# Optimization experiments

Hardware: AMD Instinct MI355X
Metric: run time of the kernel (lower is better)

The kernel has to match this reference:

```python
import jax, jax.numpy as jnp
import numpy as np

B, S, D = 2, 2048, 1024
H, KS = 16, 64

def setup_inputs() -> dict:
    key = jax.random.key(0)
    k1, k2, k3, k4, k5 = jax.random.split(key, 5)
    return {
        "x": jax.random.normal(k1, (B, S, D), dtype=jnp.float32),
        "Wq": jax.random.normal(k2, (D, KS, H), dtype=jnp.float32) * 0.02,
        "Wk": jax.random.normal(k3, (D, KS, H), dtype=jnp.float32) * 0.02,
        "Wv": jax.random.normal(k4, (D, KS, H), dtype=jnp.float32) * 0.02,
        "kernel": jax.random.normal(k5, (H * KS, KS), dtype=jnp.float32) * 0.02,
    }

def reference(x, Wq, Wk, Wv, kernel):
    b, s, d = x.shape
    ks, h = Wq.shape[1], Wq.shape[2]
    # projections: heads-last layout [b, s, ks, h]
    q = jnp.einsum('bsd,dkh->bskh', x, Wq)
    k = jnp.einsum('bsd,dkh->bskh', x, Wk)
    v = jnp.einsum('bsd,dkh->bskh', x, Wv)
    # scores [b, i(query), l(key), h]
    scores = jnp.einsum('bikh,blkh->bilh', q, k) / jnp.sqrt(jnp.float32(ks))
    # strictly-upper-triangular (future) mask, as in the original:
    # band_part(ones,0,-1) - eye  ->  1 where l > i
    li = jnp.arange(s)
    mask = (li[None, :] > li[:, None]).astype(jnp.float32)  # [s, s]
    scores = scores - 1e8 * mask[None, :, :, None]
    weights = jax.nn.softmax(scores, axis=2)  # softmax over key axis l
    heads = jnp.einsum('bilh,blkh->bikh', weights, v)  # [b, s, ks, h]
    heads = heads.reshape(b, s, ks * h)  # row-major flatten of (ks, h), matching tf.reshape
    return heads @ kernel  # [b, s, ks]
```

## Files before the change

### kernel.cpp

```cpp
#include <hip/hip_runtime.h>
#include <hip/hip_bf16.h>

#define BB 2
#define SS 2048
#define DD 1024
#define HH 16
#define KSZ 64

typedef __attribute__((ext_vector_type(8))) short s16x8;
typedef __attribute__((ext_vector_type(4))) short s16x4;
typedef __attribute__((ext_vector_type(4))) float f32x4;
typedef __attribute__((ext_vector_type(8))) unsigned short u16x8;
typedef __attribute__((ext_vector_type(4))) unsigned short u16x4;
typedef __attribute__((ext_vector_type(2))) unsigned int u32x2;
typedef unsigned short u16;

__device__ __forceinline__ u16 bf16rne(float f) {
  unsigned int u = __float_as_uint(f);
  unsigned int r = (u + 0x7FFFu + ((u >> 16) & 1u)) >> 16;
  return (u16)r;
}

__device__ __forceinline__ unsigned int cvtpk_bf16(float lo, float hi) {
  unsigned int r;
  asm("v_cvt_pk_bf16_f32 %0, %1, %2" : "=v"(r) : "v"(lo), "v"(hi));
  return r;
}

#if __has_builtin(__builtin_amdgcn_mfma_f32_16x16x16_bf16)
__device__ __forceinline__ f32x4 mfma16(s16x4 a, s16x4 b, f32x4 c) {
  return __builtin_amdgcn_mfma_f32_16x16x16_bf16(a, b, c, 0, 0, 0);
}
#elif __has_builtin(__builtin_amdgcn_mfma_f32_16x16x16bf16_1k)
__device__ __forceinline__ f32x4 mfma16(s16x4 a, s16x4 b, f32x4 c) {
  return __builtin_amdgcn_mfma_f32_16x16x16bf16_1k(a, b, c, 0, 0, 0);
}
#else
__device__ __forceinline__ f32x4 mfma16(s16x4 a, s16x4 b, f32x4 c) {
  asm("s_nop 1\n\tv_mfma_f32_16x16x16_bf16 %0, %1, %2, %0"
      : "+v"(c) : "v"(a), "v"(b));
  return c;
}
#endif

__device__ __forceinline__ void lds_dma16(const u16* g, u16* l) {
  __builtin_amdgcn_global_load_lds(
      (const __attribute__((address_space(1))) unsigned int*)(const void*)g,
      (__attribute__((address_space(3))) unsigned int*)(void*)l, 16, 0, 0);
}

__global__ __launch_bounds__(256) void prep_all(
    const float* __restrict__ x, const float* __restrict__ Wq,
    const float* __restrict__ Wk, const float* __restrict__ Wv,
    const float* __restrict__ kern, u16* __restrict__ xb,
    u16* __restrict__ Wt, u16* __restrict__ BpT) {
  __shared__ float Ts[64][65];
  const int bid = blockIdx.x;
  const int tid = threadIdx.x;
  if (bid < 2048) {
    int idx = (bid * 256 + tid) * 8;
    float4 a = *(const float4*)(x + idx);
    float4 b = *(const float4*)(x + idx + 4);
    u16x8 v;
    v[0] = bf16rne(a.x); v[1] = bf16rne(a.y); v[2] = bf16rne(a.z); v[3] = bf16rne(a.w);
    v[4] = bf16rne(b.x); v[5] = bf16rne(b.y); v[6] = bf16rne(b.z); v[7] = bf16rne(b.w);
    *(u16x8*)(xb + idx) = v;
  } else if (bid < 2816) {
    const int bx = bid - 2048;
    const int p = bx >> 8, rem = bx & 255;
    const int d0 = (rem & 15) * 64, n0 = (rem >> 4) * 64;
    const float* W = (p == 0) ? Wq : (p == 1) ? Wk : Wv;
    u16* Wo = Wt + (size_t)p * DD * DD;
    #pragma unroll
    for (int i = 0; i < 4; ++i) {
      int f4 = tid + i * 256;
      int r = f4 >> 4, c4 = f4 & 15;
      float4 v = *(const float4*)(W + (size_t)(d0 + r) * DD + n0 + c4 * 4);
      Ts[r][c4 * 4 + 0] = v.x; Ts[r][c4 * 4 + 1] = v.y;
      Ts[r][c4 * 4 + 2] = v.z; Ts[r][c4 * 4 + 3] = v.w;
    }
    __syncthreads();
    #pragma unroll
    for (int i = 0; i < 4; ++i) {
      int ch = tid + i * 256;
      int n = ch >> 4, d4 = ch & 15;
      u16x4 o;
      #pragma unroll
      for (int j = 0; j < 4; ++j) o[j] = bf16rne(Ts[d4 * 4 + j][n]);
      *(u16x4*)(Wo + (size_t)(n0 + n) * DD + d0 + d4 * 4) = o;
    }
  } else {
    const int n = bid - 2816;
    const int k4 = tid * 4;
    u16x4 o;
    #pragma unroll
    for (int j = 0; j < 4; ++j) {
      int kp = k4 + j;
      int h = kp >> 6, k = kp & 63;
      o[j] = bf16rne(kern[(size_t)(k * HH + h) * KSZ + n]);
    }
    *(u16x4*)(BpT + (size_t)n * (HH * KSZ) + k4) = o;
  }
}

__global__ __launch_bounds__(512, 6) void proj_kernel(
    const u16* __restrict__ xb, const u16* __restrict__ Wt,
    u16* __restrict__ qkvT) {
  const int xcd = blockIdx.x & 7;
  const int idx = blockIdx.x >> 3;
  const int mt = (xcd >> 1) * 8 + (idx & 7);
  const int nt = (xcd & 1) * 4 + ((idx >> 3) & 3);
  const int p  = idx >> 5;
  const int m0 = mt * 128, n0 = nt * 128;
  const u16* W = Wt + (size_t)p * DD * DD;
  u16* outp = qkvT + (size_t)p * (BB * HH * SS * KSZ);

  __shared__ __align__(16) unsigned char raw[49152];
  u16* lds = (u16*)raw;
  u16* Cs  = (u16*)raw;

  const int tid = threadIdx.x;
  const int wave = tid >> 6, lane = tid & 63;
  const int g = lane >> 4, c = lane & 15;
  const int mbase = (wave & 1) * 64, nbase = (wave >> 1) * 32;

  const int lr = lane >> 2, lc = lane & 3;
  const int swz = (lc ^ ((lr >> 1) & 3)) * 8;
  const int rS = wave * 16;
  const u16* srcA = xb + (size_t)(m0 + rS + lr) * DD + swz;
  const u16* srcB = W  + (size_t)(n0 + rS + lr) * DD + swz;
  const int sl = rS * 32;

  f32x4 acc[4][2];
  #pragma unroll
  for (int i = 0; i < 4; ++i)
    #pragma unroll
    for (int j = 0; j < 2; ++j) acc[i][j] = {0.f, 0.f, 0.f, 0.f};

  {
    u16* A0 = lds;                u16* B0 = lds + 4096;
    u16* A1 = lds + 8192;         u16* B1 = lds + 8192 + 4096;
    lds_dma16(srcA, A0 + sl);       lds_dma16(srcB, B0 + sl);
    lds_dma16(srcA + 32, A1 + sl);  lds_dma16(srcB + 32, B1 + sl);
  }

  const int jsw = (c >> 1) & 3;
  int cr = 0;
  #pragma unroll 1
  for (int t = 0; t < 31; ++t) {
    asm volatile("s_waitcnt vmcnt(2)" ::: "memory");
    __builtin_amdgcn_s_barrier();
    __builtin_amdgcn_sched_barrier(0);
    if (t <= 29) {
      const int st = cr ? cr - 1 : 2;
      const int ko = (t + 2) * 32;
      u16* An = lds + st * 8192;
      u16* Bn = An + 4096;
      lds_dma16(srcA + ko, An + sl);  lds_dma16(srcB + ko, Bn + sl);
    }
    u16* Ac = lds + cr * 8192;
    u16* Bc = Ac + 4096;
    s16x8 af[4], bfr[2];
    #pragma unroll
    for (int mf = 0; mf < 4; ++mf)
      af[mf] = *(const s16x8*)&Ac[(mbase + mf * 16 + c) * 32 + ((g ^ jsw) * 8)];
    #pragma unroll
    for (int nf = 0; nf < 2; ++nf)
      bfr[nf] = *(const s16x8*)&Bc[(nbase + nf * 16 + c) * 32 + ((g ^ jsw) * 8)];
    #pragma unroll
    for (int mf = 0; mf < 4; ++mf)
      #pragma unroll
      for (int nf = 0; nf < 2; ++nf)
        acc[mf][nf] = __builtin_amdgcn_mfma_f32_16x16x32_bf16(
            af[mf], bfr[nf], acc[mf][nf], 0, 0, 0);
    cr = (cr >= 2) ? 0 : cr + 1;
  }
  asm volatile("s_waitcnt vmcnt(0)" ::: "memory");
  __builtin_amdgcn_s_barrier();
  __builtin_amdgcn_sched_barrier(0);
  {
    u16* Ac = lds + cr * 8192;
    u16* Bc = Ac + 4096;
    s16x8 af[4], bfr[2];
    #pragma unroll
    for (int mf = 0; mf < 4; ++mf)
      af[mf] = *(const s16x8*)&Ac[(mbase + mf * 16 + c) * 32 + ((g ^ jsw) * 8)];
    #pragma unroll
    for (int nf = 0; nf < 2; ++nf)
      bfr[nf] = *(const s16x8*)&Bc[(nbase + nf * 16 + c) * 32 + ((g ^ jsw) * 8)];
    #pragma unroll
    for (int mf = 0; mf < 4; ++mf)
      #pragma unroll
      for (int nf = 0; nf < 2; ++nf)
        acc[mf][nf] = __builtin_amdgcn_mfma_f32_16x16x32_bf16(
            af[mf], bfr[nf], acc[mf][nf], 0, 0, 0);
  }
  __syncthreads();

  const float cscale = (p == 0) ? 0.125f * 1.44269504f : 1.0f;
  #pragma unroll
  for (int mf = 0; mf < 4; ++mf)
    #pragma unroll
    for (int nf = 0; nf < 2; ++nf)
      #pragma unroll
      for (int r = 0; r < 4; ++r)
        Cs[(mbase + mf * 16 + g * 4 + r) * 136 + nbase + nf * 16 + c] =
            bf16rne(acc[mf][nf][r] * cscale);
  __syncthreads();
  const int b = m0 >> 11;
  if (p < 2) {
    int hh = tid >> 5, s5 = tid & 31;
    #pragma unroll
    for (int i = 0; i < 4; ++i) {
      int row = i * 32 + s5;
      int s = (m0 + row) & 2047;
      u16x8 v;
      #pragma unroll
      for (int kp = 0; kp < 8; ++kp) v[kp] = Cs[row * 136 + kp * 16 + hh];
      *(u16x8*)(outp + ((size_t)(b * HH + hh) * SS + s) * KSZ + (n0 >> 4)) = v;
    }
  } else {
    const int s0 = m0 & 2047;
    #pragma unroll
    for (int i = 0; i < 4; ++i) {
      int chunk = tid + i * 512;
      int colid = chunk >> 4;
      int hh = colid >> 3, kp = colid & 7;
      int s8 = chunk & 15;
      u16x8 v;
      #pragma unroll
      for (int j = 0; j < 8; ++j) v[j] = Cs[(s8 * 8 + j) * 136 + kp * 16 + hh];
      *(u16x8*)(outp + ((size_t)(b * HH + hh) * KSZ + (n0 >> 4) + kp) * SS +
                s0 + s8 * 8) = v;
    }
  }
}

__global__ __launch_bounds__(256, 2) void attn_kernel(
    const u16* __restrict__ qkvT, u16* __restrict__ headsB) {
  const int bid = blockIdx.x;
  const int hb = bid & 31;
  const int q5 = bid >> 5;
  const int qt = (q5 < 8) ? q5 : 23 - q5;
  const int h = hb & 15, b = hb >> 4;
  const size_t plane = (size_t)(b * HH + h) * SS * KSZ;
  const size_t PSZ = (size_t)BB * HH * SS * KSZ;
  const u16* Qg = qkvT + plane;
  const u16* Kg = qkvT + PSZ + plane;
  const u16* Vg = qkvT + 2 * PSZ + plane;

  __shared__ u16 Ks[2][64 * 64];
  __shared__ u16 Vt[2][64 * 64];

  const int tid = threadIdx.x;
  const int lane = tid & 63;
  const int g = lane >> 4, c = lane & 15;
  const int wq0 = (tid >> 6) * 32;
  const int sr = tid >> 3, sc = tid & 7;
  const int soA = sr * 64 + ((sc ^ (sr & 7)) * 8);
  const int soB = soA + 32 * 64;

  const int nt = 2 * qt + 2;

  s16x8 bq[2][2];
  #pragma unroll
  for (int sq = 0; sq < 2; ++sq) {
    const size_t qrow = (size_t)(qt * 128 + wq0 + sq * 16 + c) * KSZ;
    bq[sq][0] = *(const s16x8*)(Qg + qrow + g * 8);
    bq[sq][1] = *(const s16x8*)(Qg + qrow + 32 + g * 8);
  }

  u16x8 kr0 = *(const u16x8*)(Kg + (size_t)sr * KSZ + sc * 8);
  u16x8 kr1 = *(const u16x8*)(Kg + (size_t)(sr + 32) * KSZ + sc * 8);
  u16x8 vr0 = *(const u16x8*)(Vg + (size_t)sr * SS + sc * 8);
  u16x8 vr1 = *(const u16x8*)(Vg + (size_t)(sr + 32) * SS + sc * 8);
  *(u16x8*)&Ks[0][soA] = kr0; *(u16x8*)&Ks[0][soB] = kr1;
  *(u16x8*)&Vt[0][soA] = vr0; *(u16x8*)&Vt[0][soB] = vr1;
  kr0 = *(const u16x8*)(Kg + (size_t)(64 + sr) * KSZ + sc * 8);
  kr1 = *(const u16x8*)(Kg + (size_t)(64 + sr + 32) * KSZ + sc * 8);
  vr0 = *(const u16x8*)(Vg + (size_t)sr * SS + 64 + sc * 8);
  vr1 = *(const u16x8*)(Vg + (size_t)(sr + 32) * SS + 64 + sc * 8);
  __syncthreads();

  f32x4 o[2][4];
  #pragma unroll
  for (int sq = 0; sq < 2; ++sq)
    #pragma unroll
    for (int mf = 0; mf < 4; ++mf) o[sq][mf] = {0.f, 0.f, 0.f, 0.f};
  float l_i[2] = {0.f, 0.f};
  const int cswz = c & 7;

  #pragma unroll 1
  for (int t = 0; t < nt; ++t) {
    const int buf = t & 1;
    if (t + 1 < nt) {
      const int nb = buf ^ 1;
      *(u16x8*)&Ks[nb][soA] = kr0; *(u16x8*)&Ks[nb][soB] = kr1;
      *(u16x8*)&Vt[nb][soA] = vr0; *(u16x8*)&Vt[nb][soB] = vr1;
      if (t + 2 < nt) {
        const int kv2 = t + 2;
        kr0 = *(const u16x8*)(Kg + (size_t)(kv2 * 64 + sr) * KSZ + sc * 8);
        kr1 = *(const u16x8*)(Kg + (size_t)(kv2 * 64 + sr + 32) * KSZ + sc * 8);
        vr0 = *(const u16x8*)(Vg + (size_t)sr * SS + kv2 * 64 + sc * 8);
        vr1 = *(const u16x8*)(Vg + (size_t)(sr + 32) * SS + kv2 * 64 + sc * 8);
      }
    }
    f32x4 s[2][4];
    #pragma unroll
    for (int sq = 0; sq < 2; ++sq)
      #pragma unroll
      for (int mf = 0; mf < 4; ++mf) s[sq][mf] = {0.f, 0.f, 0.f, 0.f};
    __builtin_amdgcn_s_setprio(1);
    #pragma unroll
    for (int ks = 0; ks < 2; ++ks) {
      #pragma unroll
      for (int mf = 0; mf < 4; ++mf) {
        s16x8 ak = *(const s16x8*)&Ks[buf][(mf * 16 + c) * 64 +
                                          (((ks * 4 + g) ^ cswz) * 8)];
        s[0][mf] = __builtin_amdgcn_mfma_f32_16x16x32_bf16(ak, bq[0][ks],
                                                           s[0][mf], 0, 0, 0);
        s[1][mf] = __builtin_amdgcn_mfma_f32_16x16x32_bf16(ak, bq[1][ks],
                                                           s[1][mf], 0, 0, 0);
      }
    }
    __builtin_amdgcn_s_setprio(0);
    if (t >= 2 * qt) {
      const int rel = (t - 2 * qt) * 64;
      #pragma unroll
      for (int sq = 0; sq < 2; ++sq) {
        const int qloc = wq0 + sq * 16 + c;
        #pragma unroll
        for (int mf = 0; mf < 4; ++mf)
          #pragma unroll
          for (int r = 0; r < 4; ++r)
            if (rel + mf * 16 + g * 4 + r > qloc) s[sq][mf][r] = -1e30f;
      }
    }
    s16x4 bp[2][4];
    #pragma unroll
    for (int sq = 0; sq < 2; ++sq) {
      #pragma unroll
      for (int mf = 0; mf < 4; ++mf) {
        float p0 = __builtin_amdgcn_exp2f(s[sq][mf][0]);
        float p1 = __builtin_amdgcn_exp2f(s[sq][mf][1]);
        float p2 = __builtin_amdgcn_exp2f(s[sq][mf][2]);
        float p3 = __builtin_amdgcn_exp2f(s[sq][mf][3]);
        l_i[sq] += (p0 + p1) + (p2 + p3);
        u32x2 pk;
        pk[0] = cvtpk_bf16(p0, p1);
        pk[1] = cvtpk_bf16(p2, p3);
        bp[sq][mf] = __builtin_bit_cast(s16x4, pk);
      }
    }
    __builtin_amdgcn_s_setprio(1);
    #pragma unroll
    for (int mf = 0; mf < 4; ++mf) {
      #pragma unroll
      for (int kb = 0; kb < 4; ++kb) {
        s16x4 av = *(const s16x4*)&Vt[buf][(mf * 16 + c) * 64 +
                                           (((kb * 2 + (g >> 1)) ^ cswz) * 8) +
                                           (g & 1) * 4];
        o[0][mf] = mfma16(av, bp[0][kb], o[0][mf]);
        o[1][mf] = mfma16(av, bp[1][kb], o[1][mf]);
      }
    }
    __builtin_amdgcn_s_setprio(0);
    __syncthreads();
  }
  #pragma unroll
  for (int sq = 0; sq < 2; ++sq) {
    float l = l_i[sq];
    l += __shfl_xor(l, 16);
    l += __shfl_xor(l, 32);
    const float inv = 1.0f / l;
    const int q = qt * 128 + wq0 + sq * 16 + c;
    #pragma unroll
    for (int mf = 0; mf < 4; ++mf) {
      u16x4 hv;
      #pragma unroll
      for (int r = 0; r < 4; ++r) hv[r] = bf16rne(o[sq][mf][r] * inv);
      *(u16x4*)(headsB + plane + (size_t)q * KSZ + mf * 16 + g * 4) = hv;
    }
  }
}

__global__ __launch_bounds__(256) void out_kernel(
    const u16* __restrict__ headsB, const u16* __restrict__ BpT,
    float* __restrict__ out) {
  const int m0 = blockIdx.x * 16;
  const int tid = threadIdx.x;
  const int wave = tid >> 6, lane = tid & 63;
  const int g = lane >> 4, c = lane & 15;

  const int m = m0 + c;
  const int b = m >> 11, s = m & 2047;

  f32x4 acc[4];
  #pragma unroll
  for (int nf = 0; nf < 4; ++nf) acc[nf] = {0.f, 0.f, 0.f, 0.f};

  #pragma unroll
  for (int it = 0; it < 8; ++it) {
    const int kb = wave * 256 + it * 32;
    const int hh = kb >> 6, kk = (kb & 63) + g * 8;
    s16x8 a = *(const s16x8*)(headsB +
        ((size_t)(b * HH + hh) * SS + s) * KSZ + kk);
    #pragma unroll
    for (int nf = 0; nf < 4; ++nf) {
      s16x8 bf = *(const s16x8*)(BpT +
          (size_t)(nf * 16 + c) * (HH * KSZ) + kb + g * 8);
      acc[nf] = __builtin_amdgcn_mfma_f32_16x16x32_bf16(a, bf, acc[nf], 0, 0, 0);
    }
  }

  __shared__ __align__(16) float red[4][64][16];
  #pragma unroll
  for (int nf = 0; nf < 4; ++nf)
    *(f32x4*)&red[wave][lane][nf * 4] = acc[nf];
  __syncthreads();

  const int mi = tid >> 4, n4 = (tid & 15) * 4;
  const int gg = mi >> 2, rr = mi & 3;
  float4 res;
  float* rp = &res.x;
  #pragma unroll
  for (int j = 0; j < 4; ++j) {
    int n = n4 + j;
    int cc = n & 15, nf = n >> 4;
    rp[j] = red[0][gg * 16 + cc][nf * 4 + rr] + red[1][gg * 16 + cc][nf * 4 + rr] +
            red[2][gg * 16 + cc][nf * 4 + rr] + red[3][gg * 16 + cc][nf * 4 + rr];
  }
  *(float4*)(out + (size_t)(m0 + mi) * KSZ + n4) = res;
}

extern "C" void kernel_launch(void* const* d_in, const int* in_sizes, int n_in,
                              void* d_out, int out_size, void* d_ws, size_t ws_size,
                              hipStream_t stream) {
  const float* x    = (const float*)d_in[0];
  const float* Wq   = (const float*)d_in[1];
  const float* Wk   = (const float*)d_in[2];
  const float* Wv   = (const float*)d_in[3];
  const float* kern = (const float*)d_in[4];
  float* out = (float*)d_out;

  u16* xb     = (u16*)d_ws;
  u16* Wt     = xb + (size_t)4096 * 1024;
  u16* qkvT   = Wt + (size_t)3 * 1024 * 1024;
  u16* headsB = qkvT + (size_t)3 * BB * HH * SS * KSZ;
  u16* BpT    = headsB + (size_t)BB * HH * SS * KSZ;

  prep_all<<<dim3(2880), 256, 0, stream>>>(x, Wq, Wk, Wv, kern, xb, Wt, BpT);
  proj_kernel<<<dim3(768), 512, 0, stream>>>(xb, Wt, qkvT);
  attn_kernel<<<dim3(512), 256, 0, stream>>>(qkvT, headsB);
  out_kernel<<<dim3(256), 256, 0, stream>>>(headsB, BpT, out);
}
```

Before: 157.0 us.

## Enlarge projection GEMM tiles to 256x256 with two-pass epilogue

The QKV projection GEMM now uses 256x256 output tiles per 512-thread block instead of 128x128. That quadruples the register accumulators per wave and doubles LDS staging, cutting global reloads of A and B. The grid shrinks from 768 to 192 blocks, which drops the XCD-aware block swizzle and leaves fewer blocks than CUs on a 256-CU MI355X. The epilogue writes back through LDS in two 128-row halves to fit the store buffer. Risks are underfilled CUs, lower occupancy, and register pressure from 128 accumulator floats per lane.

```diff
diff --git a/kernel.cpp b/kernel.cpp
--- a/kernel.cpp
+++ b/kernel.cpp
@@ -103,74 +103,78 @@
   }
 }
 
-__global__ __launch_bounds__(512, 6) void proj_kernel(
+__global__ __launch_bounds__(512, 2) void proj_kernel(
     const u16* __restrict__ xb, const u16* __restrict__ Wt,
     u16* __restrict__ qkvT) {
-  const int xcd = blockIdx.x & 7;
-  const int idx = blockIdx.x >> 3;
-  const int mt = (xcd >> 1) * 8 + (idx & 7);
-  const int nt = (xcd & 1) * 4 + ((idx >> 3) & 3);
-  const int p  = idx >> 5;
-  const int m0 = mt * 128, n0 = nt * 128;
+  const int bid = blockIdx.x;
+  const int p   = bid >> 6;
+  const int rem = bid & 63;
+  const int mt  = rem & 15, nt = rem >> 4;
+  const int m0 = mt * 256, n0 = nt * 256;
   const u16* W = Wt + (size_t)p * DD * DD;
   u16* outp = qkvT + (size_t)p * (BB * HH * SS * KSZ);
 
-  __shared__ __align__(16) unsigned char raw[49152];
+  __shared__ __align__(16) unsigned char raw[98304];
   u16* lds = (u16*)raw;
   u16* Cs  = (u16*)raw;
 
   const int tid = threadIdx.x;
   const int wave = tid >> 6, lane = tid & 63;
   const int g = lane >> 4, c = lane & 15;
-  const int mbase = (wave & 1) * 64, nbase = (wave >> 1) * 32;
+  const int mbase = (wave & 1) * 128, nbase = (wave >> 1) * 64;
 
   const int lr = lane >> 2, lc = lane & 3;
   const int swz = (lc ^ ((lr >> 1) & 3)) * 8;
-  const int rS = wave * 16;
-  const u16* srcA = xb + (size_t)(m0 + rS + lr) * DD + swz;
-  const u16* srcB = W  + (size_t)(n0 + rS + lr) * DD + swz;
-  const int sl = rS * 32;
-
-  f32x4 acc[4][2];
-  #pragma unroll
-  for (int i = 0; i < 4; ++i)
-    #pragma unroll
-    for (int j = 0; j < 2; ++j) acc[i][j] = {0.f, 0.f, 0.f, 0.f};
+  const int rA0 = wave * 32, rA1 = wave * 32 + 16;
+  const u16* srcA0 = xb + (size_t)(m0 + rA0 + lr) * DD + swz;
+  const u16* srcA1 = xb + (size_t)(m0 + rA1 + lr) * DD + swz;
+  const u16* srcB0 = W  + (size_t)(n0 + rA0 + lr) * DD + swz;
+  const u16* srcB1 = W  + (size_t)(n0 + rA1 + lr) * DD + swz;
+  const int sl0 = rA0 * 32, sl1 = rA1 * 32;
+
+  f32x4 acc[8][4];
+  #pragma unroll
+  for (int i = 0; i < 8; ++i)
+    #pragma unroll
+    for (int j = 0; j < 4; ++j) acc[i][j] = {0.f, 0.f, 0.f, 0.f};
 
   {
-    u16* A0 = lds;                u16* B0 = lds + 4096;
-    u16* A1 = lds + 8192;         u16* B1 = lds + 8192 + 4096;
-    lds_dma16(srcA, A0 + sl);       lds_dma16(srcB, B0 + sl);
-    lds_dma16(srcA + 32, A1 + sl);  lds_dma16(srcB + 32, B1 + sl);
+    u16* A0 = lds;                 u16* B0 = lds + 8192;
+    u16* A1 = lds + 16384;         u16* B1 = lds + 16384 + 8192;
+    lds_dma16(srcA0, A0 + sl0);       lds_dma16(srcA1, A0 + sl1);
+    lds_dma16(srcB0, B0 + sl0);       lds_dma16(srcB1, B0 + sl1);
+    lds_dma16(srcA0 + 32, A1 + sl0);  lds_dma16(srcA1 + 32, A1 + sl1);
+    lds_dma16(srcB0 + 32, B1 + sl0);  lds_dma16(srcB1 + 32, B1 + sl1);
   }
 
   const int jsw = (c >> 1) & 3;
   int cr = 0;
   #pragma unroll 1
   for (int t = 0; t < 31; ++t) {
-    asm volatile("s_waitcnt vmcnt(2)" ::: "memory");
+    asm volatile("s_waitcnt vmcnt(4)" ::: "memory");
     __builtin_amdgcn_s_barrier();
     __builtin_amdgcn_sched_barrier(0);
     if (t <= 29) {
       const int st = cr ? cr - 1 : 2;
       const int ko = (t + 2) * 32;
-      u16* An = lds + st * 8192;
-      u16* Bn = An + 4096;
-      lds_dma16(srcA + ko, An + sl);  lds_dma16(srcB + ko, Bn + sl);
-    }
-    u16* Ac = lds + cr * 8192;
-    u16* Bc = Ac + 4096;
-    s16x8 af[4], bfr[2];
-    #pragma unroll
-    for (int mf = 0; mf < 4; ++mf)
+      u16* An = lds + st * 16384;
+      u16* Bn = An + 8192;
+      lds_dma16(srcA0 + ko, An + sl0);  lds_dma16(srcA1 + ko, An + sl1);
+      lds_dma16(srcB0 + ko, Bn + sl0);  lds_dma16(srcB1 + ko, Bn + sl1);
+    }
+    u16* Ac = lds + cr * 16384;
+    u16* Bc = Ac + 8192;
+    s16x8 af[8], bfr[4];
+    #pragma unroll
+    for (int mf = 0; mf < 8; ++mf)
       af[mf] = *(const s16x8*)&Ac[(mbase + mf * 16 + c) * 32 + ((g ^ jsw) * 8)];
     #pragma unroll
-    for (int nf = 0; nf < 2; ++nf)
+    for (int nf = 0; nf < 4; ++nf)
       bfr[nf] = *(const s16x8*)&Bc[(nbase + nf * 16 + c) * 32 + ((g ^ jsw) * 8)];
     #pragma unroll
-    for (int mf = 0; mf < 4; ++mf)
-      #pragma unroll
-      for (int nf = 0; nf < 2; ++nf)
+    for (int mf = 0; mf < 8; ++mf)
+      #pragma unroll
+      for (int nf = 0; nf < 4; ++nf)
         acc[mf][nf] = __builtin_amdgcn_mfma_f32_16x16x32_bf16(
             af[mf], bfr[nf], acc[mf][nf], 0, 0, 0);
     cr = (cr >= 2) ? 0 : cr + 1;
@@ -179,59 +183,65 @@
   __builtin_amdgcn_s_barrier();
   __builtin_amdgcn_sched_barrier(0);
   {
-    u16* Ac = lds + cr * 8192;
-    u16* Bc = Ac + 4096;
-    s16x8 af[4], bfr[2];
-    #pragma unroll
-    for (int mf = 0; mf < 4; ++mf)
+    u16* Ac = lds + cr * 16384;
+    u16* Bc = Ac + 8192;
+    s16x8 af[8], bfr[4];
+    #pragma unroll
+    for (int mf = 0; mf < 8; ++mf)
       af[mf] = *(const s16x8*)&Ac[(mbase + mf * 16 + c) * 32 + ((g ^ jsw) * 8)];
     #pragma unroll
-    for (int nf = 0; nf < 2; ++nf)
+    for (int nf = 0; nf < 4; ++nf)
       bfr[nf] = *(const s16x8*)&Bc[(nbase + nf * 16 + c) * 32 + ((g ^ jsw) * 8)];
     #pragma unroll
-    for (int mf = 0; mf < 4; ++mf)
-      #pragma unroll
-      for (int nf = 0; nf < 2; ++nf)
+    for (int mf = 0; mf < 8; ++mf)
+      #pragma unroll
+      for (int nf = 0; nf < 4; ++nf)
         acc[mf][nf] = __builtin_amdgcn_mfma_f32_16x16x32_bf16(
             af[mf], bfr[nf], acc[mf][nf], 0, 0, 0);
   }
-  __syncthreads();
 
   const float cscale = (p == 0) ? 0.125f * 1.44269504f : 1.0f;
-  #pragma unroll
-  for (int mf = 0; mf < 4; ++mf)
-    #pragma unroll
-    for (int nf = 0; nf < 2; ++nf)
-      #pragma unroll
-      for (int r = 0; r < 4; ++r)
-        Cs[(mbase + mf * 16 + g * 4 + r) * 136 + nbase + nf * 16 + c] =
-            bf16rne(acc[mf][nf][r] * cscale);
-  __syncthreads();
-  const int b = m0 >> 11;
-  if (p < 2) {
-    int hh = tid >> 5, s5 = tid & 31;
-    #pragma unroll
-    for (int i = 0; i < 4; ++i) {
-      int row = i * 32 + s5;
-      int s = (m0 + row) & 2047;
-      u16x8 v;
-      #pragma unroll
-      for (int kp = 0; kp < 8; ++kp) v[kp] = Cs[row * 136 + kp * 16 + hh];
-      *(u16x8*)(outp + ((size_t)(b * HH + hh) * SS + s) * KSZ + (n0 >> 4)) = v;
-    }
-  } else {
-    const int s0 = m0 & 2047;
-    #pragma unroll
-    for (int i = 0; i < 4; ++i) {
-      int chunk = tid + i * 512;
-      int colid = chunk >> 4;
-      int hh = colid >> 3, kp = colid & 7;
-      int s8 = chunk & 15;
-      u16x8 v;
-      #pragma unroll
-      for (int j = 0; j < 8; ++j) v[j] = Cs[(s8 * 8 + j) * 136 + kp * 16 + hh];
-      *(u16x8*)(outp + ((size_t)(b * HH + hh) * KSZ + (n0 >> 4) + kp) * SS +
-                s0 + s8 * 8) = v;
+  #pragma unroll 1
+  for (int hhalf = 0; hhalf < 2; ++hhalf) {
+    __syncthreads();
+    if ((wave & 1) == hhalf) {
+      #pragma unroll
+      for (int mf = 0; mf < 8; ++mf)
+        #pragma unroll
+        for (int nf = 0; nf < 4; ++nf)
+          #pragma unroll
+          for (int r = 0; r < 4; ++r)
+            Cs[(mf * 16 + g * 4 + r) * 264 + nbase + nf * 16 + c] =
+                bf16rne(acc[mf][nf][r] * cscale);
+    }
+    __syncthreads();
+    const int rowg = m0 + hhalf * 128;
+    const int bb = rowg >> 11;
+    if (p < 2) {
+      #pragma unroll
+      for (int i = 0; i < 8; ++i) {
+        int idx = tid + i * 512;
+        int hh = idx & 15, kq = (idx >> 4) & 1, row = idx >> 5;
+        int s = (rowg + row) & 2047;
+        u16x8 v;
+        #pragma unroll
+        for (int j = 0; j < 8; ++j) v[j] = Cs[row * 264 + (kq * 8 + j) * 16 + hh];
+        *(u16x8*)(outp + ((size_t)(bb * HH + hh) * SS + s) * KSZ +
+                  (n0 >> 4) + kq * 8) = v;
+      }
+    } else {
+      const int s0 = rowg & 2047;
+      #pragma unroll
+      for (int i = 0; i < 8; ++i) {
+        int idx = tid + i * 512;
+        int col = idx & 255, s8 = idx >> 8;
+        int hh = col & 15, kk = col >> 4;
+        u16x8 v;
+        #pragma unroll
+        for (int j = 0; j < 8; ++j) v[j] = Cs[(s8 * 8 + j) * 264 + col];
+        *(u16x8*)(outp + ((size_t)(bb * HH + hh) * KSZ + (n0 >> 4) + kk) * SS +
+                  s0 + s8 * 8) = v;
+      }
     }
   }
 }
@@ -450,7 +460,7 @@
   u16* BpT    = headsB + (size_t)BB * HH * SS * KSZ;
 
   prep_all<<<dim3(2880), 256, 0, stream>>>(x, Wq, Wk, Wv, kern, xb, Wt, BpT);
-  proj_kernel<<<dim3(768), 512, 0, stream>>>(xb, Wt, qkvT);
+  proj_kernel<<<dim3(192), 512, 0, stream>>>(xb, Wt, qkvT);
   attn_kernel<<<dim3(512), 256, 0, stream>>>(qkvT, headsB);
   out_kernel<<<dim3(256), 256, 0, stream>>>(headsB, BpT, out);
 }
```

Measured after the change: 161.4 us. 2.8% more time.
